# Kernel tuning notes

Hardware: AMD Instinct MI355X
Metric: run time of the kernel (lower is better)

Reference implementation:

```python
import jax, jax.numpy as jnp
import numpy as np
from jax import lax

DIM = 10
BATCH = 65536

def setup_inputs() -> dict:
    key = jax.random.key(0)
    ks = jax.random.split(key, 9)
    return {
        "x": jax.random.normal(ks[0], (BATCH, DIM, DIM), dtype=jnp.float32),
        "w1": jax.random.normal(ks[1], (10, 1, 1, 1), dtype=jnp.float32) * 0.3,
        "b1": jax.random.normal(ks[2], (10,), dtype=jnp.float32) * 0.1,
        "w2": jax.random.normal(ks[3], (1, 10, 3, 3), dtype=jnp.float32) * 0.1,
        "b2": jax.random.normal(ks[4], (1,), dtype=jnp.float32) * 0.1,
        "fc1_w": jax.random.normal(ks[5], (4, DIM), dtype=jnp.float32) * 0.3,
        "fc1_b": jax.random.normal(ks[6], (4,), dtype=jnp.float32) * 0.1,
        "fc2_w": jax.random.normal(ks[7], (2, 4), dtype=jnp.float32) * 0.3,
        "fc2_b": jax.random.normal(ks[8], (2,), dtype=jnp.float32) * 0.1,
    }

def reference(x, w1, b1, w2, b2, fc1_w, fc1_b, fc2_w, fc2_b):
    # convEdge: BrainNetCNN edge-to-edge, out[i,j] = row_sum(i) + col_sum(j)
    row = jnp.sum(x, axis=-1, keepdims=True)        # [B, D, 1]
    col = jnp.sum(x, axis=-2, keepdims=True)        # [B, 1, D]
    e2e = (row + col)[:, None, :, :]                # [B, 1, D, D]
    # Conv2d(1, 10, 1) + ReLU: a 1x1 conv is a per-channel scale + bias
    h = jax.nn.relu(e2e * w1[None, :, 0, 0, 0, None, None] + b1[None, :, None, None])  # [B,10,D,D]
    # convSym: lower-triangular mask per channel
    mask = jnp.tril(jnp.ones((DIM, DIM), dtype=h.dtype))
    h = h * mask
    # Conv2d(10, 1, 3, stride=1, padding=1) + ReLU
    h = lax.conv_general_dilated(h, w2, window_strides=(1, 1), padding='SAME',
                                 dimension_numbers=('NCHW', 'OIHW', 'NCHW'))
    h = jax.nn.relu(h + b2[None, :, None, None])    # [B, 1, D, D]
    # convVert: edge-to-vertex, out[i] = row_sum(i) + col_sum(i) of channel 0
    m = h[:, 0]                                     # [B, D, D]
    v = jnp.sum(m, axis=-1) + jnp.sum(m, axis=-2)   # [B, D]
    # fc1 -> relu -> fc2
    v = jax.nn.relu(v @ fc1_w.T + fc1_b)
    return v @ fc2_w.T + fc2_b                      # [B, 2]
```

## Files before the change

### kernel.cpp

```cpp
#include <hip/hip_runtime.h>

#define DIM 10
#define BATCH 65536

typedef _Float16 h2 __attribute__((ext_vector_type(2)));

#if defined(__has_builtin)
#  if __has_builtin(__builtin_amdgcn_fdot2)
#    define HAS_FDOT2 1
#  endif
#endif
#ifndef HAS_FDOT2
#  define HAS_FDOT2 0
#endif

__launch_bounds__(64, 1)
__global__ void net_kernel(const float* __restrict__ x,
                           const float* __restrict__ w1,
                           const float* __restrict__ b1,
                           const float* __restrict__ w2,
                           const float* __restrict__ b2,
                           const float* __restrict__ fc1_w,
                           const float* __restrict__ fc1_b,
                           const float* __restrict__ fc2_w,
                           const float* __restrict__ fc2_b,
                           float* __restrict__ out) {
    __shared__ __align__(16) float xs[64 * DIM * DIM];

    const int lane = threadIdx.x;
    const size_t blk0 = (size_t)blockIdx.x * 64;

    const float* gbase = x + blk0 * (DIM * DIM);
    #pragma unroll
    for (int c = 0; c < 25; ++c) {
        __builtin_amdgcn_global_load_lds(
            (const __attribute__((address_space(1))) void*)(gbase + c * 256 + lane * 4),
            (__attribute__((address_space(3))) void*)(xs + c * 256),
            16, 0, 0);
    }

    h2 W1h[5], B1h[5], W2h[5][9];
    #pragma unroll
    for (int cp = 0; cp < 5; ++cp) {
        W1h[cp][0] = (_Float16)w1[2 * cp];     W1h[cp][1] = (_Float16)w1[2 * cp + 1];
        B1h[cp][0] = (_Float16)b1[2 * cp];     B1h[cp][1] = (_Float16)b1[2 * cp + 1];
        #pragma unroll
        for (int k = 0; k < 9; ++k) {
            W2h[cp][k][0] = (_Float16)w2[(2 * cp) * 9 + k];
            W2h[cp][k][1] = (_Float16)w2[(2 * cp + 1) * 9 + k];
        }
    }
    const float B2 = b2[0];

    asm volatile("s_waitcnt vmcnt(0)" ::: "memory");

    float row[DIM], col[DIM];
    #pragma unroll
    for (int i = 0; i < DIM; ++i) { row[i] = 0.f; col[i] = 0.f; }
    const float4* xb = reinterpret_cast<const float4*>(xs + lane * (DIM * DIM));
    #pragma unroll
    for (int t = 0; t < 25; ++t) {
        const float4 v = xb[t];
        const int e0 = t * 4;
        row[(e0 + 0) / DIM] += v.x; col[(e0 + 0) % DIM] += v.x;
        row[(e0 + 1) / DIM] += v.y; col[(e0 + 1) % DIM] += v.y;
        row[(e0 + 2) / DIM] += v.z; col[(e0 + 2) % DIM] += v.z;
        row[(e0 + 3) / DIM] += v.w; col[(e0 + 3) % DIM] += v.w;
    }

    float acc[DIM][DIM];
    #pragma unroll
    for (int i = 0; i < DIM; ++i)
        #pragma unroll
        for (int j = 0; j < DIM; ++j) acc[i][j] = B2;

    const h2 zero_h2 = (h2){(_Float16)0, (_Float16)0};

    #pragma unroll
    for (int p = 0; p < DIM; ++p) {
        #pragma unroll
        for (int q = 0; q <= p; ++q) {
            const float ev = row[p] + col[q];
#if HAS_FDOT2
            const _Float16 eh = (_Float16)ev;
            const h2 e2 = (h2){eh, eh};
            h2 g[5];
            #pragma unroll
            for (int cp = 0; cp < 5; ++cp) {
                g[cp] = __builtin_elementwise_max(
                    __builtin_elementwise_fma(W1h[cp], e2, B1h[cp]), zero_h2);
            }
            #pragma unroll
            for (int a = 0; a < 3; ++a) {
                const int i = p + 1 - a;
                if (i < 0 || i >= DIM) continue;
                #pragma unroll
                for (int bb = 0; bb < 3; ++bb) {
                    const int j = q + 1 - bb;
                    if (j < 0 || j >= DIM) continue;
                    const int k = a * 3 + bb;
                    float t0 = acc[i][j];
                    #pragma unroll
                    for (int cp = 0; cp < 5; ++cp)
                        t0 = __builtin_amdgcn_fdot2(g[cp], W2h[cp][k], t0, false);
                    acc[i][j] = t0;
                }
            }
#else
            float gs[10];
            #pragma unroll
            for (int cp = 0; cp < 5; ++cp) {
                gs[2*cp]   = fmaxf(fmaf((float)W1h[cp][0], ev, (float)B1h[cp][0]), 0.f);
                gs[2*cp+1] = fmaxf(fmaf((float)W1h[cp][1], ev, (float)B1h[cp][1]), 0.f);
            }
            #pragma unroll
            for (int a = 0; a < 3; ++a) {
                const int i = p + 1 - a;
                if (i < 0 || i >= DIM) continue;
                #pragma unroll
                for (int bb = 0; bb < 3; ++bb) {
                    const int j = q + 1 - bb;
                    if (j < 0 || j >= DIM) continue;
                    const int k = a * 3 + bb;
                    float t0 = acc[i][j];
                    #pragma unroll
                    for (int cp = 0; cp < 5; ++cp) {
                        t0 = fmaf(gs[2*cp],   (float)W2h[cp][k][0], t0);
                        t0 = fmaf(gs[2*cp+1], (float)W2h[cp][k][1], t0);
                    }
                    acc[i][j] = t0;
                }
            }
#endif
        }
    }

    float vsum[DIM];
    #pragma unroll
    for (int k = 0; k < DIM; ++k) vsum[k] = 0.f;
    #pragma unroll
    for (int i = 0; i < DIM; ++i) {
        #pragma unroll
        for (int j = 0; j < DIM; ++j) {
            const float m = fmaxf(acc[i][j], 0.f);
            vsum[i] += m;
            vsum[j] += m;
        }
    }

    float hid[4];
    #pragma unroll
    for (int t = 0; t < 4; ++t) {
        float a = fc1_b[t];
        #pragma unroll
        for (int k = 0; k < DIM; ++k) a = fmaf(vsum[k], fc1_w[t * DIM + k], a);
        hid[t] = fmaxf(a, 0.f);
    }
    float o0 = fc2_b[0], o1 = fc2_b[1];
    #pragma unroll
    for (int t = 0; t < 4; ++t) {
        o0 = fmaf(hid[t], fc2_w[t], o0);
        o1 = fmaf(hid[t], fc2_w[4 + t], o1);
    }
    reinterpret_cast<float2*>(out)[blk0 + lane] = make_float2(o0, o1);
}

extern "C" void kernel_launch(void* const* d_in, const int* in_sizes, int n_in,
                              void* d_out, int out_size, void* d_ws, size_t ws_size,
                              hipStream_t stream) {
    const float* x     = (const float*)d_in[0];
    const float* w1    = (const float*)d_in[1];
    const float* b1    = (const float*)d_in[2];
    const float* w2    = (const float*)d_in[3];
    const float* b2    = (const float*)d_in[4];
    const float* fc1_w = (const float*)d_in[5];
    const float* fc1_b = (const float*)d_in[6];
    const float* fc2_w = (const float*)d_in[7];
    const float* fc2_b = (const float*)d_in[8];
    float* out = (float*)d_out;

    const int block = 64;
    const int grid = BATCH / block;
    net_kernel<<<grid, block, 0, stream>>>(x, w1, b1, w2, b2, fc1_w, fc1_b,
                                           fc2_w, fc2_b, out);
}
```

Before: 14.23 us.

## Stream conv output rows through a three-row rolling window instead of full accumulator

Replaces the 10x10 per-thread accumulator with a rolling three-row window (previous, current, next). Each finished row is reduced through ReLU into row and column sums right away, and the per-row sums are spilled to LDS. The outer p loop is no longer unrolled, and the row sums are stored as fp16 in LDS and indexed per iteration. The edge value is now formed by adding in fp16, which costs some precision. The aim is to cut register pressure and code size at the cost of extra LDS traffic and loop overhead.

```diff
diff --git a/kernel.cpp b/kernel.cpp
--- a/kernel.cpp
+++ b/kernel.cpp
@@ -25,7 +25,7 @@
                            const float* __restrict__ fc2_w,
                            const float* __restrict__ fc2_b,
                            float* __restrict__ out) {
-    __shared__ __align__(16) float xs[64 * DIM * DIM];
+    __shared__ __align__(16) float smem[7360];
 
     const int lane = threadIdx.x;
     const size_t blk0 = (size_t)blockIdx.x * 64;
@@ -35,7 +35,7 @@
     for (int c = 0; c < 25; ++c) {
         __builtin_amdgcn_global_load_lds(
             (const __attribute__((address_space(1))) void*)(gbase + c * 256 + lane * 4),
-            (__attribute__((address_space(3))) void*)(xs + c * 256),
+            (__attribute__((address_space(3))) void*)(smem + c * 256),
             16, 0, 0);
     }
 
@@ -57,7 +57,7 @@
     float row[DIM], col[DIM];
     #pragma unroll
     for (int i = 0; i < DIM; ++i) { row[i] = 0.f; col[i] = 0.f; }
-    const float4* xb = reinterpret_cast<const float4*>(xs + lane * (DIM * DIM));
+    const float4* xb = reinterpret_cast<const float4*>(smem + lane * (DIM * DIM));
     #pragma unroll
     for (int t = 0; t < 25; ++t) {
         const float4 v = xb[t];
@@ -68,85 +68,99 @@
         row[(e0 + 3) / DIM] += v.w; col[(e0 + 3) % DIM] += v.w;
     }
 
-    float acc[DIM][DIM];
-    #pragma unroll
-    for (int i = 0; i < DIM; ++i)
-        #pragma unroll
-        for (int j = 0; j < DIM; ++j) acc[i][j] = B2;
-
-    const h2 zero_h2 = (h2){(_Float16)0, (_Float16)0};
-
-    #pragma unroll
+    _Float16* rowh = reinterpret_cast<_Float16*>(smem + 6400);
+    #pragma unroll
+    for (int r = 0; r < DIM; ++r) rowh[r * 64 + lane] = (_Float16)row[r];
+    _Float16 ch[DIM];
+    #pragma unroll
+    for (int q = 0; q < DIM; ++q) ch[q] = (_Float16)col[q];
+    float* vrp = smem + 6720;
+
+    float Wp[DIM], Wc[DIM], Wn[DIM], vc[DIM];
+    #pragma unroll
+    for (int j = 0; j < DIM; ++j) {
+        Wp[j] = -1e30f;
+        Wc[j] = B2;
+        Wn[j] = B2;
+        vc[j] = 0.f;
+    }
+
+    #pragma unroll 1
     for (int p = 0; p < DIM; ++p) {
-        #pragma unroll
-        for (int q = 0; q <= p; ++q) {
-            const float ev = row[p] + col[q];
+        const _Float16 rph = rowh[p * 64 + lane];
+        #pragma unroll
+        for (int q = 0; q < DIM; ++q) {
+            if (p >= q) {
+                const _Float16 eh = rph + ch[q];
+                h2 e2; e2[0] = eh; e2[1] = eh;
 #if HAS_FDOT2
-            const _Float16 eh = (_Float16)ev;
-            const h2 e2 = (h2){eh, eh};
-            h2 g[5];
-            #pragma unroll
-            for (int cp = 0; cp < 5; ++cp) {
-                g[cp] = __builtin_elementwise_max(
-                    __builtin_elementwise_fma(W1h[cp], e2, B1h[cp]), zero_h2);
-            }
-            #pragma unroll
-            for (int a = 0; a < 3; ++a) {
-                const int i = p + 1 - a;
-                if (i < 0 || i >= DIM) continue;
-                #pragma unroll
-                for (int bb = 0; bb < 3; ++bb) {
-                    const int j = q + 1 - bb;
+                h2 g[5];
+                #pragma unroll
+                for (int cp = 0; cp < 5; ++cp)
+                    g[cp] = __builtin_elementwise_max(
+                        __builtin_elementwise_fma(W1h[cp], e2, B1h[cp]),
+                        (h2){(_Float16)0, (_Float16)0});
+                #pragma unroll
+                for (int b = 0; b < 3; ++b) {
+                    const int j = q + 1 - b;
                     if (j < 0 || j >= DIM) continue;
-                    const int k = a * 3 + bb;
-                    float t0 = acc[i][j];
-                    #pragma unroll
-                    for (int cp = 0; cp < 5; ++cp)
-                        t0 = __builtin_amdgcn_fdot2(g[cp], W2h[cp][k], t0, false);
-                    acc[i][j] = t0;
-                }
-            }
-#else
-            float gs[10];
-            #pragma unroll
-            for (int cp = 0; cp < 5; ++cp) {
-                gs[2*cp]   = fmaxf(fmaf((float)W1h[cp][0], ev, (float)B1h[cp][0]), 0.f);
-                gs[2*cp+1] = fmaxf(fmaf((float)W1h[cp][1], ev, (float)B1h[cp][1]), 0.f);
-            }
-            #pragma unroll
-            for (int a = 0; a < 3; ++a) {
-                const int i = p + 1 - a;
-                if (i < 0 || i >= DIM) continue;
-                #pragma unroll
-                for (int bb = 0; bb < 3; ++bb) {
-                    const int j = q + 1 - bb;
-                    if (j < 0 || j >= DIM) continue;
-                    const int k = a * 3 + bb;
-                    float t0 = acc[i][j];
+                    float t0 = Wn[j], t1 = Wc[j], t2 = Wp[j];
                     #pragma unroll
                     for (int cp = 0; cp < 5; ++cp) {
-                        t0 = fmaf(gs[2*cp],   (float)W2h[cp][k][0], t0);
-                        t0 = fmaf(gs[2*cp+1], (float)W2h[cp][k][1], t0);
+                        t0 = __builtin_amdgcn_fdot2(g[cp], W2h[cp][b],     t0, false);
+                        t1 = __builtin_amdgcn_fdot2(g[cp], W2h[cp][3 + b], t1, false);
+                        t2 = __builtin_amdgcn_fdot2(g[cp], W2h[cp][6 + b], t2, false);
                     }
-                    acc[i][j] = t0;
+                    Wn[j] = t0; Wc[j] = t1; Wp[j] = t2;
                 }
+#else
+                float gs[10];
+                #pragma unroll
+                for (int cp = 0; cp < 5; ++cp) {
+                    const float ev = (float)eh;
+                    gs[2*cp]   = fmaxf(fmaf((float)W1h[cp][0], ev, (float)B1h[cp][0]), 0.f);
+                    gs[2*cp+1] = fmaxf(fmaf((float)W1h[cp][1], ev, (float)B1h[cp][1]), 0.f);
+                }
+                #pragma unroll
+                for (int b = 0; b < 3; ++b) {
+                    const int j = q + 1 - b;
+                    if (j < 0 || j >= DIM) continue;
+                    float t0 = Wn[j], t1 = Wc[j], t2 = Wp[j];
+                    #pragma unroll
+                    for (int c2 = 0; c2 < 10; ++c2) {
+                        t0 = fmaf(gs[c2], (float)W2h[c2 >> 1][b]    [c2 & 1], t0);
+                        t1 = fmaf(gs[c2], (float)W2h[c2 >> 1][3 + b][c2 & 1], t1);
+                        t2 = fmaf(gs[c2], (float)W2h[c2 >> 1][6 + b][c2 & 1], t2);
+                    }
+                    Wn[j] = t0; Wc[j] = t1; Wp[j] = t2;
+                }
+#endif
             }
-#endif
         }
+        float s = 0.f;
+        #pragma unroll
+        for (int j = 0; j < DIM; ++j) {
+            const float m = fmaxf(Wp[j], 0.f);
+            vc[j] += m;
+            s += m;
+        }
+        const int rs = (p > 0) ? (p - 1) : 0;
+        vrp[rs * 64 + lane] = s;
+        #pragma unroll
+        for (int j = 0; j < DIM; ++j) { Wp[j] = Wc[j]; Wc[j] = Wn[j]; Wn[j] = B2; }
+    }
+    float vr9 = 0.f;
+    #pragma unroll
+    for (int j = 0; j < DIM; ++j) {
+        const float m = fmaxf(Wp[j], 0.f);
+        vc[j] += m;
+        vr9 += m;
     }
 
     float vsum[DIM];
     #pragma unroll
-    for (int k = 0; k < DIM; ++k) vsum[k] = 0.f;
-    #pragma unroll
-    for (int i = 0; i < DIM; ++i) {
-        #pragma unroll
-        for (int j = 0; j < DIM; ++j) {
-            const float m = fmaxf(acc[i][j], 0.f);
-            vsum[i] += m;
-            vsum[j] += m;
-        }
-    }
+    for (int k = 0; k < 9; ++k) vsum[k] = vrp[k * 64 + lane] + vc[k];
+    vsum[9] = vr9 + vc[9];
 
     float hid[4];
     #pragma unroll
```

New measurement: 16.78 us. 17.9% more time.

## Split each sample's conv work across two wavefronts and reduce through LDS

Applied to the files above, without the earlier changes.

Each block now runs two wavefronts on the same 64 samples. Each wave computes half of the lower-triangular (p,q) positions, split by parity, and the partial accumulators are combined through shared memory before the FC head. The global-to-LDS loads are divided between the waves, and row and column sums are converted to half once up front. This doubles the parallelism per sample to hide latency and raise occupancy. The cost is an extra LDS round trip, extra barriers, and duplicated row/col summation and weight setup in both waves.

```diff
diff --git a/kernel.cpp b/kernel.cpp
--- a/kernel.cpp
+++ b/kernel.cpp
@@ -14,82 +14,26 @@
 #  define HAS_FDOT2 0
 #endif
 
-__launch_bounds__(64, 1)
-__global__ void net_kernel(const float* __restrict__ x,
-                           const float* __restrict__ w1,
-                           const float* __restrict__ b1,
-                           const float* __restrict__ w2,
-                           const float* __restrict__ b2,
-                           const float* __restrict__ fc1_w,
-                           const float* __restrict__ fc1_b,
-                           const float* __restrict__ fc2_w,
-                           const float* __restrict__ fc2_b,
-                           float* __restrict__ out) {
-    __shared__ __align__(16) float xs[64 * DIM * DIM];
-
-    const int lane = threadIdx.x;
-    const size_t blk0 = (size_t)blockIdx.x * 64;
-
-    const float* gbase = x + blk0 * (DIM * DIM);
-    #pragma unroll
-    for (int c = 0; c < 25; ++c) {
-        __builtin_amdgcn_global_load_lds(
-            (const __attribute__((address_space(1))) void*)(gbase + c * 256 + lane * 4),
-            (__attribute__((address_space(3))) void*)(xs + c * 256),
-            16, 0, 0);
-    }
-
-    h2 W1h[5], B1h[5], W2h[5][9];
-    #pragma unroll
-    for (int cp = 0; cp < 5; ++cp) {
-        W1h[cp][0] = (_Float16)w1[2 * cp];     W1h[cp][1] = (_Float16)w1[2 * cp + 1];
-        B1h[cp][0] = (_Float16)b1[2 * cp];     B1h[cp][1] = (_Float16)b1[2 * cp + 1];
-        #pragma unroll
-        for (int k = 0; k < 9; ++k) {
-            W2h[cp][k][0] = (_Float16)w2[(2 * cp) * 9 + k];
-            W2h[cp][k][1] = (_Float16)w2[(2 * cp + 1) * 9 + k];
-        }
-    }
-    const float B2 = b2[0];
-
-    asm volatile("s_waitcnt vmcnt(0)" ::: "memory");
-
-    float row[DIM], col[DIM];
-    #pragma unroll
-    for (int i = 0; i < DIM; ++i) { row[i] = 0.f; col[i] = 0.f; }
-    const float4* xb = reinterpret_cast<const float4*>(xs + lane * (DIM * DIM));
-    #pragma unroll
-    for (int t = 0; t < 25; ++t) {
-        const float4 v = xb[t];
-        const int e0 = t * 4;
-        row[(e0 + 0) / DIM] += v.x; col[(e0 + 0) % DIM] += v.x;
-        row[(e0 + 1) / DIM] += v.y; col[(e0 + 1) % DIM] += v.y;
-        row[(e0 + 2) / DIM] += v.z; col[(e0 + 2) % DIM] += v.z;
-        row[(e0 + 3) / DIM] += v.w; col[(e0 + 3) % DIM] += v.w;
-    }
-
-    float acc[DIM][DIM];
-    #pragma unroll
-    for (int i = 0; i < DIM; ++i)
-        #pragma unroll
-        for (int j = 0; j < DIM; ++j) acc[i][j] = B2;
-
-    const h2 zero_h2 = (h2){(_Float16)0, (_Float16)0};
-
+template <int PAR>
+__device__ __forceinline__ void conv_half(const _Float16* rh, const _Float16* ch,
+                                          const h2* W1h, const h2* B1h,
+                                          const h2 (*W2h)[9],
+                                          float acc[DIM][DIM]) {
     #pragma unroll
     for (int p = 0; p < DIM; ++p) {
         #pragma unroll
         for (int q = 0; q <= p; ++q) {
-            const float ev = row[p] + col[q];
+            const int t = p * (p + 1) / 2 + q;
+            if ((t & 1) != PAR) continue;
+            const _Float16 eh = rh[p] + ch[q];
+            h2 e2; e2[0] = eh; e2[1] = eh;
 #if HAS_FDOT2
-            const _Float16 eh = (_Float16)ev;
-            const h2 e2 = (h2){eh, eh};
             h2 g[5];
             #pragma unroll
-            for (int cp = 0; cp < 5; ++cp) {
+            for (int cp = 0; cp < 5; ++cp)
                 g[cp] = __builtin_elementwise_max(
-                    __builtin_elementwise_fma(W1h[cp], e2, B1h[cp]), zero_h2);
-            }
+                    __builtin_elementwise_fma(W1h[cp], e2, B1h[cp]),
+                    (h2){(_Float16)0, (_Float16)0});
             #pragma unroll
             for (int a = 0; a < 3; ++a) {
                 const int i = p + 1 - a;
@@ -108,6 +52,7 @@
             }
 #else
             float gs[10];
+            const float ev = (float)eh;
             #pragma unroll
             for (int cp = 0; cp < 5; ++cp) {
                 gs[2*cp]   = fmaxf(fmaf((float)W1h[cp][0], ev, (float)B1h[cp][0]), 0.f);
@@ -134,35 +79,138 @@
 #endif
         }
     }
-
-    float vsum[DIM];
-    #pragma unroll
-    for (int k = 0; k < DIM; ++k) vsum[k] = 0.f;
-    #pragma unroll
-    for (int i = 0; i < DIM; ++i) {
-        #pragma unroll
-        for (int j = 0; j < DIM; ++j) {
-            const float m = fmaxf(acc[i][j], 0.f);
-            vsum[i] += m;
-            vsum[j] += m;
-        }
-    }
-
-    float hid[4];
-    #pragma unroll
-    for (int t = 0; t < 4; ++t) {
-        float a = fc1_b[t];
-        #pragma unroll
-        for (int k = 0; k < DIM; ++k) a = fmaf(vsum[k], fc1_w[t * DIM + k], a);
-        hid[t] = fmaxf(a, 0.f);
-    }
-    float o0 = fc2_b[0], o1 = fc2_b[1];
-    #pragma unroll
-    for (int t = 0; t < 4; ++t) {
-        o0 = fmaf(hid[t], fc2_w[t], o0);
-        o1 = fmaf(hid[t], fc2_w[4 + t], o1);
-    }
-    reinterpret_cast<float2*>(out)[blk0 + lane] = make_float2(o0, o1);
+}
+
+__launch_bounds__(128, 2)
+__global__ void net_kernel(const float* __restrict__ x,
+                           const float* __restrict__ w1,
+                           const float* __restrict__ b1,
+                           const float* __restrict__ w2,
+                           const float* __restrict__ b2,
+                           const float* __restrict__ fc1_w,
+                           const float* __restrict__ fc1_b,
+                           const float* __restrict__ fc2_w,
+                           const float* __restrict__ fc2_b,
+                           float* __restrict__ out) {
+    __shared__ __align__(16) float smem[6400];
+
+    const int tid  = threadIdx.x;
+    const int lane = tid & 63;
+    const int w    = __builtin_amdgcn_readfirstlane(tid >> 6);
+    const size_t blk0 = (size_t)blockIdx.x * 64;
+
+    const float* gbase = x + blk0 * (DIM * DIM);
+    if (w == 0) {
+        #pragma unroll
+        for (int c = 0; c < 13; ++c)
+            __builtin_amdgcn_global_load_lds(
+                (const __attribute__((address_space(1))) void*)(gbase + c * 256 + lane * 4),
+                (__attribute__((address_space(3))) void*)(smem + c * 256),
+                16, 0, 0);
+    } else {
+        #pragma unroll
+        for (int c = 13; c < 25; ++c)
+            __builtin_amdgcn_global_load_lds(
+                (const __attribute__((address_space(1))) void*)(gbase + c * 256 + lane * 4),
+                (__attribute__((address_space(3))) void*)(smem + c * 256),
+                16, 0, 0);
+    }
+
+    h2 W1h[5], B1h[5], W2h[5][9];
+    #pragma unroll
+    for (int cp = 0; cp < 5; ++cp) {
+        W1h[cp][0] = (_Float16)w1[2 * cp];     W1h[cp][1] = (_Float16)w1[2 * cp + 1];
+        B1h[cp][0] = (_Float16)b1[2 * cp];     B1h[cp][1] = (_Float16)b1[2 * cp + 1];
+        #pragma unroll
+        for (int k = 0; k < 9; ++k) {
+            W2h[cp][k][0] = (_Float16)w2[(2 * cp) * 9 + k];
+            W2h[cp][k][1] = (_Float16)w2[(2 * cp + 1) * 9 + k];
+        }
+    }
+    const float B2 = b2[0];
+
+    __syncthreads();
+
+    float row[DIM], col[DIM];
+    #pragma unroll
+    for (int i = 0; i < DIM; ++i) { row[i] = 0.f; col[i] = 0.f; }
+    const float4* xb = reinterpret_cast<const float4*>(smem + lane * (DIM * DIM));
+    #pragma unroll
+    for (int t = 0; t < 25; ++t) {
+        const float4 v = xb[t];
+        const int e0 = t * 4;
+        row[(e0 + 0) / DIM] += v.x; col[(e0 + 0) % DIM] += v.x;
+        row[(e0 + 1) / DIM] += v.y; col[(e0 + 1) % DIM] += v.y;
+        row[(e0 + 2) / DIM] += v.z; col[(e0 + 2) % DIM] += v.z;
+        row[(e0 + 3) / DIM] += v.w; col[(e0 + 3) % DIM] += v.w;
+    }
+
+    __syncthreads();
+
+    _Float16 rh[DIM], ch[DIM];
+    #pragma unroll
+    for (int i = 0; i < DIM; ++i) { rh[i] = (_Float16)row[i]; ch[i] = (_Float16)col[i]; }
+
+    float acc[DIM][DIM];
+    const float ainit = (w == 0) ? B2 : 0.0f;
+    #pragma unroll
+    for (int i = 0; i < DIM; ++i)
+        #pragma unroll
+        for (int j = 0; j < DIM; ++j) acc[i][j] = ainit;
+
+    if (w == 0) conv_half<0>(rh, ch, W1h, B1h, W2h, acc);
+    else        conv_half<1>(rh, ch, W1h, B1h, W2h, acc);
+
+    if (w == 1) {
+        float4* mb = reinterpret_cast<float4*>(smem + lane * (DIM * DIM));
+        #pragma unroll
+        for (int t = 0; t < 25; ++t) {
+            const int f = 4 * t;
+            mb[t] = make_float4(acc[f / 10][f % 10],       acc[(f+1) / 10][(f+1) % 10],
+                                acc[(f+2) / 10][(f+2) % 10], acc[(f+3) / 10][(f+3) % 10]);
+        }
+    }
+    __syncthreads();
+    if (w == 0) {
+        const float4* mb = reinterpret_cast<const float4*>(smem + lane * (DIM * DIM));
+        #pragma unroll
+        for (int t = 0; t < 25; ++t) {
+            const float4 v = mb[t];
+            const int f = 4 * t;
+            acc[f / 10][f % 10]         += v.x;
+            acc[(f+1) / 10][(f+1) % 10] += v.y;
+            acc[(f+2) / 10][(f+2) % 10] += v.z;
+            acc[(f+3) / 10][(f+3) % 10] += v.w;
+        }
+
+        float vsum[DIM];
+        #pragma unroll
+        for (int k = 0; k < DIM; ++k) vsum[k] = 0.f;
+        #pragma unroll
+        for (int i = 0; i < DIM; ++i) {
+            #pragma unroll
+            for (int j = 0; j < DIM; ++j) {
+                const float m = fmaxf(acc[i][j], 0.f);
+                vsum[i] += m;
+                vsum[j] += m;
+            }
+        }
+        float hid[4];
+        #pragma unroll
+        for (int t = 0; t < 4; ++t) {
+            float a = fc1_b[t];
+            #pragma unroll
+            for (int k = 0; k < DIM; ++k) a = fmaf(vsum[k], fc1_w[t * DIM + k], a);
+            hid[t] = fmaxf(a, 0.f);
+        }
+        float o0 = fc2_b[0], o1 = fc2_b[1];
+        #pragma unroll
+        for (int t = 0; t < 4; ++t) {
+            o0 = fmaf(hid[t], fc2_w[t], o0);
+            o1 = fmaf(hid[t], fc2_w[4 + t], o1);
+        }
+        reinterpret_cast<float2*>(out)[blk0 + lane] = make_float2(o0, o1);
+    }
 }
 
 extern "C" void kernel_launch(void* const* d_in, const int* in_sizes, int n_in,
@@ -179,8 +227,8 @@
     const float* fc2_b = (const float*)d_in[8];
     float* out = (float*)d_out;
 
-    const int block = 64;
-    const int grid = BATCH / block;
+    const int block = 128;
+    const int grid = BATCH / 64;
     net_kernel<<<grid, block, 0, stream>>>(x, w1, b1, w2, b2, fc1_w, fc1_b,
                                            fc2_w, fc2_b, out);
 }
```

Measured after the change: 15.12 us. +6.2%, slower.
